# Kernel tuning notes

Measured on AMD Instinct MI355X. Metric: run time of the kernel, lower is better.

The kernel has to match this reference:

```python
import jax, jax.numpy as jnp
import numpy as np

EPS = 1e-6      # F.pairwise_distance adds eps to the difference vector
MARGIN = 0.2
NORM_EPS = 1e-12  # torch F.normalize clamps the norm at 1e-12


def _l2_normalize(x):
    n = jnp.linalg.norm(x, axis=1, keepdims=True)
    return x / jnp.maximum(n, NORM_EPS)


def _pairdist(A, B):
    # ||a - b + EPS||_2 for every (a, b) pair, computed without the [N,N,d] tensor:
    # ||a-b||^2 + 2*EPS*sum(a-b) + d*EPS^2
    d = A.shape[1]
    sq = (jnp.sum(A * A, axis=1)[:, None] + jnp.sum(B * B, axis=1)[None, :]
          - 2.0 * (A @ B.T)
          + 2.0 * EPS * (jnp.sum(A, axis=1)[:, None] - jnp.sum(B, axis=1)[None, :])
          + d * (EPS * EPS))
    return jnp.sqrt(jnp.maximum(sq, 0.0))


def setup_inputs() -> dict:
    key = jax.random.key(0)
    kp, kn = jax.random.split(key)
    p = jax.random.normal(kp, (8192, 128), dtype=jnp.float32)
    n = jax.random.normal(kn, (64, 128), dtype=jnp.float32)
    return {"sequence_representations_p": p, "sequence_representations_n": n}


def reference(sequence_representations_p, sequence_representations_n):
    p = _l2_normalize(sequence_representations_p)  # [l_p, d]
    n = _l2_normalize(sequence_representations_n)  # [l_n, d]
    l_p = p.shape[0]
    t = 0  # original uses random.randint(0, l_n-1); fixed for determinism
    d_pp = _pairdist(p, p)                 # [l_p, l_p]
    d_pn = _pairdist(p, n[t:t + 1])[:, 0]  # [l_p]
    distance = jnp.maximum(d_pp + MARGIN - d_pn[:, None], 0.0)
    loss = jnp.sum(distance) / ((l_p - 1) * l_p)
    return jnp.maximum(loss, 0.0)
```

## Files before the change

kernel.cpp:

```cpp
#include <hip/hip_runtime.h>
#include <hip/hip_bf16.h>

typedef float f32x16 __attribute__((ext_vector_type(16)));
typedef float f32x4v __attribute__((ext_vector_type(4)));

#define GLOBAL_AS(p) ((const __attribute__((address_space(1))) void*)(p))
#define LDS_AS(p)    ((__attribute__((address_space(3))) void*)(p))

#define LP 8192
#define D 128
#define TWOEPS 2e-6f
#define CEPS 1.28e-10f
#define MARGIN 0.2f
#define NTRI 2080
#define NBLK 512
#define INV_DENOM 1.4903545e-8f

#define BUFSZ 34816
#define AOFF 0
#define BOFF 16384
#define QWOFF 32768

__global__ __launch_bounds__(64) void rows_kernel(const float* __restrict__ p,
                                                  const float* __restrict__ n,
                                                  char* __restrict__ pb,
                                                  float* __restrict__ qw) {
    const int lane = threadIdx.x;
    const int sub = lane & 3;
    const int r = lane >> 2;
    const int row = blockIdx.x * 16 + r;

    const float4* px = (const float4*)(p + (size_t)row * D + sub * 32);
    const float4* nx = (const float4*)(n + sub * 32);
    float4 x[8], y[8];
#pragma unroll
    for (int k = 0; k < 8; ++k) { x[k] = px[k]; y[k] = nx[k]; }

    float ssp = 0.0f, ssn = 0.0f;
#pragma unroll
    for (int k = 0; k < 8; ++k) {
        ssp += fmaf(x[k].x, x[k].x, fmaf(x[k].y, x[k].y,
               fmaf(x[k].z, x[k].z, x[k].w * x[k].w)));
        ssn += fmaf(y[k].x, y[k].x, fmaf(y[k].y, y[k].y,
               fmaf(y[k].z, y[k].z, y[k].w * y[k].w)));
    }
    ssp += __shfl_xor(ssp, 1); ssp += __shfl_xor(ssp, 2);
    ssn += __shfl_xor(ssn, 1); ssn += __shfl_xor(ssn, 2);

    const float invp = 1.0f / fmaxf(sqrtf(ssp), 1e-12f);
    const float invn = 1.0f / fmaxf(sqrtf(ssn), 1e-12f);

    float s = 0.0f, q = 0.0f, dn = 0.0f, sn = 0.0f, qn = 0.0f, q8 = 0.0f;
    int pk8[8];
#pragma unroll
    for (int k = 0; k < 8; ++k) {
        float a0 = x[k].x * invp, a1 = x[k].y * invp,
              a2 = x[k].z * invp, a3 = x[k].w * invp;
        float h0 = y[k].x * invn, h1 = y[k].y * invn,
              h2 = y[k].z * invn, h3 = y[k].w * invn;
        s  += (a0 + a1) + (a2 + a3);
        q  += fmaf(a0, a0, fmaf(a1, a1, fmaf(a2, a2, a3 * a3)));
        dn += fmaf(a0, h0, fmaf(a1, h1, fmaf(a2, h2, a3 * h3)));
        sn += (h0 + h1) + (h2 + h3);
        qn += fmaf(h0, h0, fmaf(h1, h1, fmaf(h2, h2, h3 * h3)));
        int wlo = __builtin_amdgcn_cvt_pk_fp8_f32(a0, a1, 0, false);
        int wfl = __builtin_amdgcn_cvt_pk_fp8_f32(a2, a3, wlo, true);
        pk8[k] = wfl;
        float b0 = __builtin_amdgcn_cvt_f32_fp8(wfl, 0);
        float b1 = __builtin_amdgcn_cvt_f32_fp8(wfl, 1);
        float b2 = __builtin_amdgcn_cvt_f32_fp8(wfl, 2);
        float b3 = __builtin_amdgcn_cvt_f32_fp8(wfl, 3);
        q8 += fmaf(b0, b0, fmaf(b1, b1, fmaf(b2, b2, b3 * b3)));
    }
    char* dst = pb + (size_t)row * 128 + sub * 32;
    ((int4*)dst)[0] = make_int4(pk8[0], pk8[1], pk8[2], pk8[3]);
    ((int4*)dst)[1] = make_int4(pk8[4], pk8[5], pk8[6], pk8[7]);

#pragma unroll
    for (int m = 1; m < 4; m <<= 1) {
        s += __shfl_xor(s, m);
        q += __shfl_xor(q, m);
        dn += __shfl_xor(dn, m);
        sn += __shfl_xor(sn, m);
        qn += __shfl_xor(qn, m);
        q8 += __shfl_xor(q8, m);
    }
    if (sub == 0) {
        float sq = q + qn - 2.0f * dn + TWOEPS * (s - sn) + CEPS;
        float dpn = sqrtf(fmaxf(sq, 0.0f));
        *(float2*)(qw + (size_t)row * 2) = make_float2(q8, MARGIN - dpn);
    }
}

__global__ __launch_bounds__(512, 4) void pair_kernel(const char* __restrict__ pb,
                                                      const float* __restrict__ qw,
                                                      float* __restrict__ out) {
    __shared__ __align__(16) char smem[2 * BUFSZ];
    const int blk = blockIdx.x;
    const int tid = threadIdx.x;
    const int wave = tid >> 6, lane = tid & 63;
    const int nt = (blk < NTRI - 4 * NBLK) ? 5 : 4;

    const int wr = wave >> 2, wc = wave & 3;
    const int ln31 = lane & 31;
    const int h = lane >> 5;

    auto decode = [](int b, int& ti, int& tj) {
        int t = (int)((__builtin_amdgcn_sqrtf(8.0f * (float)b + 1.0f) - 1.0f) * 0.5f);
        while ((t + 1) * (t + 2) / 2 <= b) ++t;
        while (t * (t + 1) / 2 > b) --t;
        ti = t;
        tj = b - t * (t + 1) / 2;
    };

    auto stage = [&](int ti, int tj, char* buf) {
        const char* gA = pb + (size_t)ti * 128 * 128;
        const char* gB = pb + (size_t)tj * 128 * 128;
#pragma unroll
        for (int r = 0; r < 2; ++r) {
            int obase = wave * 2048 + r * 1024;
            int o = obase + lane * 16;
            int src = o ^ (((o >> 7) & 7) << 4);
            __builtin_amdgcn_global_load_lds(GLOBAL_AS(gA + src),
                                             LDS_AS(buf + AOFF + obase), 16, 0, 0);
            __builtin_amdgcn_global_load_lds(GLOBAL_AS(gB + src),
                                             LDS_AS(buf + BOFF + obase), 16, 0, 0);
        }
        int side = wave >> 2;
        int chunk = wave & 3;
        const char* gq = (const char*)qw + (size_t)(side ? tj : ti) * 1024 +
                         chunk * 256 + lane * 4;
        __builtin_amdgcn_global_load_lds(GLOBAL_AS(gq),
                                         LDS_AS(buf + QWOFF + side * 1024 + chunk * 256),
                                         4, 0, 0);
    };

    int ti0, tj0;
    decode(blk, ti0, tj0);
    stage(ti0, tj0, smem);
    bool diag_cur = (ti0 == tj0);
    bool diag_nxt = false;

    float la0 = 0.0f, la1 = 0.0f, lb0 = 0.0f, lb1 = 0.0f;

    for (int t = 0; t < nt; ++t) {
        char* cur = smem + (size_t)(t & 1) * BUFSZ;
        char* nxt = smem + (size_t)((t + 1) & 1) * BUFSZ;

        if (t + 1 < nt) {
            int ti, tj;
            decode(blk + (t + 1) * NBLK, ti, tj);
            diag_nxt = (ti == tj);
            stage(ti, tj, nxt);
            asm volatile("s_waitcnt vmcnt(5)" ::: "memory");
        } else {
            asm volatile("s_waitcnt vmcnt(0)" ::: "memory");
        }
        __builtin_amdgcn_s_barrier();
        __builtin_amdgcn_sched_barrier(0);

        const char* lA = cur + AOFF;
        const char* lB = cur + BOFF;
        const float* qwi = (const float*)(cur + QWOFF);
        const float* qwj = (const float*)(cur + QWOFF + 1024);

        f32x16 acc[2] = {};
        __builtin_amdgcn_s_setprio(1);
#pragma unroll
        for (int ks = 0; ks < 8; ++ks) {
            int co = ((ks ^ (ln31 & 7)) << 4) + h * 8;
            long bv = *(const long*)(lB + (wc * 32 + ln31) * 128 + co);
#pragma unroll
            for (int mt = 0; mt < 2; ++mt) {
                long av = *(const long*)(lA + (wr * 64 + mt * 32 + ln31) * 128 + co);
                acc[mt] = __builtin_amdgcn_mfma_f32_32x32x16_fp8_fp8(av, bv, acc[mt],
                                                                     0, 0, 0);
            }
        }
        __builtin_amdgcn_s_setprio(0);

        float2 qwjv = *(const float2*)(qwj + (wc * 32 + ln31) * 2);
        if (diag_cur) {
#pragma unroll
            for (int mt = 0; mt < 2; ++mt)
#pragma unroll
                for (int g = 0; g < 4; ++g) {
                    int rbase = wr * 64 + mt * 32 + 8 * g + 4 * h;
                    f32x4v qw01 = *(const f32x4v*)(qwi + rbase * 2);
                    f32x4v qw23 = *(const f32x4v*)(qwi + rbase * 2 + 4);
                    float qi[4] = {qw01[0], qw01[2], qw23[0], qw23[2]};
                    float wi[4] = {qw01[1], qw01[3], qw23[1], qw23[3]};
#pragma unroll
                    for (int r2 = 0; r2 < 4; ++r2) {
                        float sq = fmaf(-2.0f, acc[mt][g * 4 + r2], qi[r2] + qwjv.x);
                        float d = __builtin_amdgcn_sqrtf(fmaxf(sq, 0.0f));
                        if (mt) la1 += fmaxf(d + wi[r2], 0.0f);
                        else    la0 += fmaxf(d + wi[r2], 0.0f);
                    }
                }
        } else {
#pragma unroll
            for (int mt = 0; mt < 2; ++mt)
#pragma unroll
                for (int g = 0; g < 4; ++g) {
                    int rbase = wr * 64 + mt * 32 + 8 * g + 4 * h;
                    f32x4v qw01 = *(const f32x4v*)(qwi + rbase * 2);
                    f32x4v qw23 = *(const f32x4v*)(qwi + rbase * 2 + 4);
                    float qi[4] = {qw01[0], qw01[2], qw23[0], qw23[2]};
                    float wi[4] = {qw01[1], qw01[3], qw23[1], qw23[3]};
#pragma unroll
                    for (int r2 = 0; r2 < 4; ++r2) {
                        float sq = fmaf(-2.0f, acc[mt][g * 4 + r2], qi[r2] + qwjv.x);
                        float d = __builtin_amdgcn_sqrtf(sq);
                        if (mt) { la1 += fmaxf(d + wi[r2], 0.0f);
                                  lb1 += fmaxf(d + qwjv.y, 0.0f); }
                        else    { la0 += fmaxf(d + wi[r2], 0.0f);
                                  lb0 += fmaxf(d + qwjv.y, 0.0f); }
                    }
                }
        }
        __builtin_amdgcn_s_barrier();
        diag_cur = diag_nxt;
    }

    float local = (la0 + la1) + (lb0 + lb1);
#pragma unroll
    for (int m = 1; m < 64; m <<= 1) local += __shfl_xor(local, m);
    float* sred = (float*)smem;
    if (lane == 0) sred[wave] = local;
    __syncthreads();
    if (tid == 0) {
        float t0 = (sred[0] + sred[1]) + (sred[2] + sred[3]);
        float t1 = (sred[4] + sred[5]) + (sred[6] + sred[7]);
        atomicAdd(out, (t0 + t1) * INV_DENOM);
    }
}

extern "C" void kernel_launch(void* const* d_in, const int* in_sizes, int n_in,
                              void* d_out, int out_size, void* d_ws, size_t ws_size,
                              hipStream_t stream) {
    const float* p = (const float*)d_in[0];
    const float* n = (const float*)d_in[1];
    float* out = (float*)d_out;
    char* ws = (char*)d_ws;

    char*  pb    = ws;
    float* qwarr = (float*)(ws + (1u << 20));

    hipMemsetAsync(out, 0, sizeof(float), stream);
    hipLaunchKernelGGL(rows_kernel, dim3(LP / 16), dim3(64), 0, stream, p, n, pb, qwarr);
    hipLaunchKernelGGL(pair_kernel, dim3(NBLK), dim3(512), 0, stream, pb, qwarr, out);
}
```

Measured before the change: 32.67 us.

## Split row norms into separate arrays, load from global, fold output zeroing

The per-row q and w values move from an interleaved float2 array to two separate arrays. They are now read straight from global memory (through cache) into registers instead of being staged into LDS with global_load_lds, which shrinks the LDS buffer and drops one async load per stage. The hipMemsetAsync of the output is replaced by a store in rows_kernel, removing a separate launch. The epilogue is reshaped and setprio is dropped. The trade-off is that the epilogue now waits on global-load latency instead of LDS reads.

```diff
diff --git a/kernel.cpp b/kernel.cpp
--- a/kernel.cpp
+++ b/kernel.cpp
@@ -16,16 +16,18 @@
 #define NBLK 512
 #define INV_DENOM 1.4903545e-8f
 
-#define BUFSZ 34816
+#define BUFSZ 32768
 #define AOFF 0
 #define BOFF 16384
-#define QWOFF 32768
 
 __global__ __launch_bounds__(64) void rows_kernel(const float* __restrict__ p,
                                                   const float* __restrict__ n,
                                                   char* __restrict__ pb,
-                                                  float* __restrict__ qw) {
+                                                  float* __restrict__ qarr,
+                                                  float* __restrict__ warr,
+                                                  float* __restrict__ out) {
     const int lane = threadIdx.x;
+    if (blockIdx.x == 0 && lane == 0) out[0] = 0.0f;
     const int sub = lane & 3;
     const int r = lane >> 2;
     const int row = blockIdx.x * 16 + r;
@@ -88,12 +90,14 @@
     if (sub == 0) {
         float sq = q + qn - 2.0f * dn + TWOEPS * (s - sn) + CEPS;
         float dpn = sqrtf(fmaxf(sq, 0.0f));
-        *(float2*)(qw + (size_t)row * 2) = make_float2(q8, MARGIN - dpn);
+        qarr[row] = q8;
+        warr[row] = MARGIN - dpn;
     }
 }
 
 __global__ __launch_bounds__(512, 4) void pair_kernel(const char* __restrict__ pb,
-                                                      const float* __restrict__ qw,
+                                                      const float* __restrict__ qarr,
+                                                      const float* __restrict__ warr,
                                                       float* __restrict__ out) {
     __shared__ __align__(16) char smem[2 * BUFSZ];
     const int blk = blockIdx.x;
@@ -114,8 +118,8 @@
     };
 
     auto stage = [&](int ti, int tj, char* buf) {
-        const char* gA = pb + (size_t)ti * 128 * 128;
-        const char* gB = pb + (size_t)tj * 128 * 128;
+        const char* gA = pb + (size_t)ti * 16384;
+        const char* gB = pb + (size_t)tj * 16384;
 #pragma unroll
         for (int r = 0; r < 2; ++r) {
             int obase = wave * 2048 + r * 1024;
@@ -126,18 +130,12 @@
             __builtin_amdgcn_global_load_lds(GLOBAL_AS(gB + src),
                                              LDS_AS(buf + BOFF + obase), 16, 0, 0);
         }
-        int side = wave >> 2;
-        int chunk = wave & 3;
-        const char* gq = (const char*)qw + (size_t)(side ? tj : ti) * 1024 +
-                         chunk * 256 + lane * 4;
-        __builtin_amdgcn_global_load_lds(GLOBAL_AS(gq),
-                                         LDS_AS(buf + QWOFF + side * 1024 + chunk * 256),
-                                         4, 0, 0);
     };
 
     int ti0, tj0;
     decode(blk, ti0, tj0);
     stage(ti0, tj0, smem);
+    int icur = blk;
     bool diag_cur = (ti0 == tj0);
     bool diag_nxt = false;
 
@@ -147,80 +145,79 @@
         char* cur = smem + (size_t)(t & 1) * BUFSZ;
         char* nxt = smem + (size_t)((t + 1) & 1) * BUFSZ;
 
+        int ti, tj;
+        decode(icur, ti, tj);
+
         if (t + 1 < nt) {
-            int ti, tj;
-            decode(blk + (t + 1) * NBLK, ti, tj);
-            diag_nxt = (ti == tj);
-            stage(ti, tj, nxt);
-            asm volatile("s_waitcnt vmcnt(5)" ::: "memory");
+            int ti1, tj1;
+            decode(icur + NBLK, ti1, tj1);
+            diag_nxt = (ti1 == tj1);
+            stage(ti1, tj1, nxt);
+            asm volatile("s_waitcnt vmcnt(4)" ::: "memory");
         } else {
             asm volatile("s_waitcnt vmcnt(0)" ::: "memory");
         }
         __builtin_amdgcn_s_barrier();
         __builtin_amdgcn_sched_barrier(0);
 
+        const int i0 = ti * 128, j0 = tj * 128;
+        const int j = j0 + wc * 32 + ln31;
+        const float qj = qarr[j];
+        const float wj = warr[j];
+        f32x4v q4[2][4], w4[2][4];
+#pragma unroll
+        for (int mt = 0; mt < 2; ++mt)
+#pragma unroll
+            for (int g = 0; g < 4; ++g) {
+                int rbase = i0 + wr * 64 + mt * 32 + 8 * g + 4 * h;
+                q4[mt][g] = *(const f32x4v*)(qarr + rbase);
+                w4[mt][g] = *(const f32x4v*)(warr + rbase);
+            }
+
         const char* lA = cur + AOFF;
         const char* lB = cur + BOFF;
-        const float* qwi = (const float*)(cur + QWOFF);
-        const float* qwj = (const float*)(cur + QWOFF + 1024);
-
-        f32x16 acc[2] = {};
-        __builtin_amdgcn_s_setprio(1);
+
+        f32x16 acc0 = {}, acc1 = {};
 #pragma unroll
         for (int ks = 0; ks < 8; ++ks) {
             int co = ((ks ^ (ln31 & 7)) << 4) + h * 8;
-            long bv = *(const long*)(lB + (wc * 32 + ln31) * 128 + co);
-#pragma unroll
-            for (int mt = 0; mt < 2; ++mt) {
-                long av = *(const long*)(lA + (wr * 64 + mt * 32 + ln31) * 128 + co);
-                acc[mt] = __builtin_amdgcn_mfma_f32_32x32x16_fp8_fp8(av, bv, acc[mt],
-                                                                     0, 0, 0);
-            }
-        }
-        __builtin_amdgcn_s_setprio(0);
-
-        float2 qwjv = *(const float2*)(qwj + (wc * 32 + ln31) * 2);
+            long bv  = *(const long*)(lB + (wc * 32 + ln31) * 128 + co);
+            long av0 = *(const long*)(lA + (wr * 64 + ln31) * 128 + co);
+            long av1 = *(const long*)(lA + (wr * 64 + 32 + ln31) * 128 + co);
+            acc0 = __builtin_amdgcn_mfma_f32_32x32x16_fp8_fp8(av0, bv, acc0, 0, 0, 0);
+            acc1 = __builtin_amdgcn_mfma_f32_32x32x16_fp8_fp8(av1, bv, acc1, 0, 0, 0);
+        }
+
         if (diag_cur) {
 #pragma unroll
-            for (int mt = 0; mt < 2; ++mt)
-#pragma unroll
-                for (int g = 0; g < 4; ++g) {
-                    int rbase = wr * 64 + mt * 32 + 8 * g + 4 * h;
-                    f32x4v qw01 = *(const f32x4v*)(qwi + rbase * 2);
-                    f32x4v qw23 = *(const f32x4v*)(qwi + rbase * 2 + 4);
-                    float qi[4] = {qw01[0], qw01[2], qw23[0], qw23[2]};
-                    float wi[4] = {qw01[1], qw01[3], qw23[1], qw23[3]};
-#pragma unroll
-                    for (int r2 = 0; r2 < 4; ++r2) {
-                        float sq = fmaf(-2.0f, acc[mt][g * 4 + r2], qi[r2] + qwjv.x);
-                        float d = __builtin_amdgcn_sqrtf(fmaxf(sq, 0.0f));
-                        if (mt) la1 += fmaxf(d + wi[r2], 0.0f);
-                        else    la0 += fmaxf(d + wi[r2], 0.0f);
-                    }
+            for (int g = 0; g < 4; ++g)
+#pragma unroll
+                for (int r2 = 0; r2 < 4; ++r2) {
+                    float sq0 = fmaf(-2.0f, acc0[g * 4 + r2], q4[0][g][r2] + qj);
+                    float sq1 = fmaf(-2.0f, acc1[g * 4 + r2], q4[1][g][r2] + qj);
+                    float d0 = __builtin_amdgcn_sqrtf(fmaxf(sq0, 0.0f));
+                    float d1 = __builtin_amdgcn_sqrtf(fmaxf(sq1, 0.0f));
+                    la0 += fmaxf(d0 + w4[0][g][r2], 0.0f);
+                    la1 += fmaxf(d1 + w4[1][g][r2], 0.0f);
                 }
         } else {
 #pragma unroll
-            for (int mt = 0; mt < 2; ++mt)
-#pragma unroll
-                for (int g = 0; g < 4; ++g) {
-                    int rbase = wr * 64 + mt * 32 + 8 * g + 4 * h;
-                    f32x4v qw01 = *(const f32x4v*)(qwi + rbase * 2);
-                    f32x4v qw23 = *(const f32x4v*)(qwi + rbase * 2 + 4);
-                    float qi[4] = {qw01[0], qw01[2], qw23[0], qw23[2]};
-                    float wi[4] = {qw01[1], qw01[3], qw23[1], qw23[3]};
-#pragma unroll
-                    for (int r2 = 0; r2 < 4; ++r2) {
-                        float sq = fmaf(-2.0f, acc[mt][g * 4 + r2], qi[r2] + qwjv.x);
-                        float d = __builtin_amdgcn_sqrtf(sq);
-                        if (mt) { la1 += fmaxf(d + wi[r2], 0.0f);
-                                  lb1 += fmaxf(d + qwjv.y, 0.0f); }
-                        else    { la0 += fmaxf(d + wi[r2], 0.0f);
-                                  lb0 += fmaxf(d + qwjv.y, 0.0f); }
-                    }
+            for (int g = 0; g < 4; ++g)
+#pragma unroll
+                for (int r2 = 0; r2 < 4; ++r2) {
+                    float sq0 = fmaf(-2.0f, acc0[g * 4 + r2], q4[0][g][r2] + qj);
+                    float sq1 = fmaf(-2.0f, acc1[g * 4 + r2], q4[1][g][r2] + qj);
+                    float d0 = __builtin_amdgcn_sqrtf(sq0);
+                    float d1 = __builtin_amdgcn_sqrtf(sq1);
+                    la0 += fmaxf(d0 + w4[0][g][r2], 0.0f);
+                    la1 += fmaxf(d1 + w4[1][g][r2], 0.0f);
+                    lb0 += fmaxf(d0 + wj, 0.0f);
+                    lb1 += fmaxf(d1 + wj, 0.0f);
                 }
         }
         __builtin_amdgcn_s_barrier();
         diag_cur = diag_nxt;
+        icur += NBLK;
     }
 
     float local = (la0 + la1) + (lb0 + lb1);
@@ -244,10 +241,12 @@
     float* out = (float*)d_out;
     char* ws = (char*)d_ws;
 
-    char*  pb    = ws;
-    float* qwarr = (float*)(ws + (1u << 20));
-
-    hipMemsetAsync(out, 0, sizeof(float), stream);
-    hipLaunchKernelGGL(rows_kernel, dim3(LP / 16), dim3(64), 0, stream, p, n, pb, qwarr);
-    hipLaunchKernelGGL(pair_kernel, dim3(NBLK), dim3(512), 0, stream, pb, qwarr, out);
+    char*  pb   = ws;
+    float* qarr = (float*)(ws + (1u << 20));
+    float* warr = (float*)(ws + (1u << 20) + (32u << 10));
+
+    hipLaunchKernelGGL(rows_kernel, dim3(LP / 16), dim3(64), 0, stream, p, n, pb,
+                       qarr, warr, out);
+    hipLaunchKernelGGL(pair_kernel, dim3(NBLK), dim3(512), 0, stream, pb, qarr,
+                       warr, out);
 }
```

Measured after the change: 38.67 us. 1.18x slower.
